# Optimization experiments

Hardware: AMD Instinct MI355X
Metric: run time of the kernel (lower is better)

The kernel has to match this reference:

```python
import jax, jax.numpy as jnp
import numpy as np

B, G, C = 8, 512, 32  # batch, grid size, channel width (INIT_DIM)
NPB = 32768           # nonzeros per batch element


def _sconv(x, k, stride, pad):
    # dense conv; sparse semantics recovered by masking with the output
    # coordinate occupancy (Minkowski conv only produces active outputs)
    return jax.lax.conv_general_dilated(
        x, k, (stride, stride), [(pad, pad), (pad, pad)],
        dimension_numbers=('NHWC', 'HWIO', 'NHWC'))


def _downsample_mask(m):
    # ME strided output coord exists iff any input coord in the 2x2 cell is active
    return jax.lax.reduce_window(m, 0.0, jax.lax.max, (1, 2, 2, 1), (1, 2, 2, 1), 'VALID')


def setup_inputs() -> dict:
    key = jax.random.key(0)
    ks = jax.random.split(key, 16)
    b = jnp.repeat(jnp.arange(B, dtype=jnp.int32), NPB)
    yx = jax.random.randint(ks[0], (B * NPB, 2), 0, G, dtype=jnp.int32)
    coords = jnp.concatenate([b[:, None], yx], axis=1)          # [N,3] (b,y,x)
    feats = jax.random.normal(ks[1], (B * NPB, 1), jnp.float32)  # 1 feature/nnz
    x2 = jax.random.normal(ks[2], (B, 3), jnp.float32)
    # Minkowski conv kernels (bias=False by default); HWIO layout
    K1 = jax.random.normal(ks[3], (5, 5, 1, C), jnp.float32) * 0.28   # kaiming-ish
    K2 = jax.random.normal(ks[4], (3, 3, C, C), jnp.float32) * 0.083
    K3 = jax.random.normal(ks[5], (3, 3, C, C), jnp.float32) * 0.083
    K4 = jax.random.normal(ks[6], (3, 3, C, C), jnp.float32) * 0.083
    # feature MLP: Linear(3,64) -> ReLU -> Linear(64,32)
    W1 = jax.random.normal(ks[7], (3, 64), jnp.float32) * 0.3
    b1 = jnp.zeros((64,), jnp.float32)
    W2 = jax.random.normal(ks[8], (64, 32), jnp.float32) * 0.25
    b2 = jnp.zeros((32,), jnp.float32)
    # matrix_embedding: Linear(64,128) -> ReLU
    W3 = jax.random.normal(ks[9], (64, 128), jnp.float32) * 0.18
    b3 = jnp.zeros((128,), jnp.float32)
    return {'coords': coords, 'feats': feats, 'x2': x2,
            'K1': K1, 'K2': K2, 'K3': K3, 'K4': K4,
            'W1': W1, 'b1': b1, 'W2': W2, 'b2': b2, 'W3': W3, 'b3': b3}


def reference(coords, feats, x2, K1, K2, K3, K4, W1, b1, W2, b2, W3, b3):
    bi, yi, xi = coords[:, 0], coords[:, 1], coords[:, 2]
    grid = jnp.zeros((B, G, G, 1), jnp.float32).at[bi, yi, xi, 0].set(feats[:, 0])
    m1 = jnp.zeros((B, G, G, 1), jnp.float32).at[bi, yi, xi, 0].set(1.0)
    # layer1: k=5 s=1 (output coords == input coords)
    y1 = jax.nn.relu(_sconv(grid, K1, 1, 2)) * m1
    # layers 2-4: k=3 s=2; centered at even positions, masked by strided occupancy
    m2 = _downsample_mask(m1)
    y2 = jax.nn.relu(_sconv(y1, K2, 2, 1)) * m2
    m3 = _downsample_mask(m2)
    y3 = jax.nn.relu(_sconv(y2, K3, 2, 1)) * m3
    m4 = _downsample_mask(m3)
    y4 = jax.nn.relu(_sconv(y3, K4, 2, 1)) * m4
    # global average pool over active output coordinates per batch
    cnt = jnp.sum(m4, axis=(1, 2))                      # [B,1]
    pooled = jnp.sum(y4, axis=(1, 2)) / jnp.maximum(cnt, 1.0)  # [B,32]
    # aux feature MLP
    h = jax.nn.relu(x2[:, :3] @ W1 + b1) @ W2 + b2      # [B,32]
    z = jnp.concatenate([pooled, h], axis=1)            # [B,64]
    return jax.nn.relu(z @ W3 + b3)                     # [B,128]
```

## Files before the change

kernel.cpp:

```cpp
#include <hip/hip_runtime.h>
#include <hip/hip_bf16.h>
#include <stdint.h>


static constexpr int G_ = 512;
static constexpr int NPTS = 8 * 32768;

#define DEVI __device__ __forceinline__

typedef __attribute__((ext_vector_type(8))) short bf16x8;
typedef __attribute__((ext_vector_type(4))) float f32x4;
typedef __attribute__((ext_vector_type(4))) unsigned u32x4;

DEVI float bf_lo(unsigned w) { return __uint_as_float(w << 16); }
DEVI float bf_hi(unsigned w) { return __uint_as_float(w & 0xFFFF0000u); }
DEVI unsigned comp(const uint4& v, int i) {
  return i == 0 ? v.x : i == 1 ? v.y : i == 2 ? v.z : v.w;
}
DEVI unsigned short f2bf_bits(float f) {
  unsigned u = __float_as_uint(f);
  unsigned r = u + 0x7FFFu + ((u >> 16) & 1u);
  return (unsigned short)(r >> 16);
}

__global__ __launch_bounds__(256) void k_scatter(const int* __restrict__ coords,
                                                 int* __restrict__ idxg) {
  int i = blockIdx.x * 256 + threadIdx.x;
  if (i >= NPTS) return;
  int b = coords[3 * i], y = coords[3 * i + 1], x = coords[3 * i + 2];
  atomicMax(&idxg[((size_t)b * G_ + y) * G_ + x], i);
}

__global__ __launch_bounds__(256) void k_grid(const int* __restrict__ idxg,
                                              const float* __restrict__ feats,
                                              unsigned* __restrict__ grid2) {
  int i = blockIdx.x * 256 + threadIdx.x;
  int v = idxg[i];
  float f = (v >= 0) ? feats[v] : 0.0f;
  unsigned short hb = f2bf_bits(f);
  unsigned short lb = f2bf_bits(f - __uint_as_float((unsigned)hb << 16));
  grid2[i] = (unsigned)hb | ((unsigned)lb << 16);
}

__global__ __launch_bounds__(256) void k_packw(
    const float* __restrict__ K1f, const float* __restrict__ K2,
    const float* __restrict__ K3, const float* __restrict__ K4,
    unsigned short* __restrict__ pw1h, unsigned short* __restrict__ pw1l,
    unsigned short* __restrict__ pw2, unsigned short* __restrict__ pw3,
    unsigned short* __restrict__ pw4) {
  const int t = threadIdx.x;
  if (t < 128) {
    int h = t >> 6, ln = t & 63;
    int g2 = ln >> 4, co = h * 16 + (ln & 15);
#pragma unroll
    for (int j = 0; j < 8; j++) {
      int k = 8 * g2 + j;
      float v = (k < 25) ? K1f[k * 32 + co] : 0.f;
      unsigned short hb = f2bf_bits(v);
      pw1h[t * 8 + j] = hb;
      pw1l[t * 8 + j] = f2bf_bits(v - __uint_as_float((unsigned)hb << 16));
    }
  }
  const float* Ks[3] = {K2, K3, K4};
  unsigned short* ps[3] = {pw2, pw3, pw4};
  for (int m = 0; m < 3; m++)
    for (int e = t; e < 1152; e += 256) {
      int kk = e >> 7, rem = e & 127;
      int h = rem >> 6, ln = rem & 63;
      int g2 = ln >> 4, co = h * 16 + (ln & 15);
#pragma unroll
      for (int j = 0; j < 8; j++)
        ps[m][e * 8 + j] = f2bf_bits(Ks[m][((kk * 32) + 8 * g2 + j) * 32 + co]);
    }
}

__global__ __launch_bounds__(256) void k_masks(const int* __restrict__ idxg,
                                               float* __restrict__ m2,
                                               float* __restrict__ m3,
                                               float* __restrict__ m4) {
  __shared__ float sm2[32][32];
  __shared__ float sm3[16][16];
  const int b = blockIdx.z, ty0 = blockIdx.y * 32, tx0 = blockIdx.x * 32;
  const int t = threadIdx.x;
  for (int i = t; i < 1024; i += 256) {
    int r = i >> 5, c = i & 31;
    const int* p = idxg + ((size_t)b * 512 + 2 * (ty0 + r)) * 512 + 2 * (tx0 + c);
    float v = ((p[0] & p[1] & p[512] & p[513]) >= 0) ? 1.f : 0.f;
    m2[((size_t)b * 256 + ty0 + r) * 256 + tx0 + c] = v;
    sm2[r][c] = v;
  }
  __syncthreads();
  {
    int r = t >> 4, c = t & 15;
    float v = fmaxf(fmaxf(sm2[2 * r][2 * c], sm2[2 * r][2 * c + 1]),
                    fmaxf(sm2[2 * r + 1][2 * c], sm2[2 * r + 1][2 * c + 1]));
    m3[((size_t)b * 128 + (ty0 >> 1) + r) * 128 + (tx0 >> 1) + c] = v;
    sm3[r][c] = v;
  }
  __syncthreads();
  if (t < 64) {
    int r = t >> 3, c = t & 7;
    float v = fmaxf(fmaxf(sm3[2 * r][2 * c], sm3[2 * r][2 * c + 1]),
                    fmaxf(sm3[2 * r + 1][2 * c], sm3[2 * r + 1][2 * c + 1]));
    m4[((size_t)b * 64 + (ty0 >> 2) + r) * 64 + (tx0 >> 2) + c] = v;
  }
}

__global__ __launch_bounds__(256) void k_conv1_mfma(
    const unsigned* __restrict__ grid2, const int* __restrict__ idxg,
    const unsigned short* __restrict__ pw1h,
    const unsigned short* __restrict__ pw1l,
    __hip_bfloat16* __restrict__ y1) {
  constexpr int PITCH = 264;
  __shared__ unsigned s_tile[8 * PITCH];
  const int t = threadIdx.x;
  const int b = blockIdx.z, R = blockIdx.y * 4, x0 = blockIdx.x * 256;
  for (int i = t; i < 8 * 260; i += 256) {
    int rr = i / 260, cc = i - rr * 260;
    int gy = R - 2 + rr, gx = x0 - 2 + cc;
    unsigned v = 0;
    if (gy >= 0 && gy < G_ && gx >= 0 && gx < G_)
      v = grid2[((size_t)b * G_ + gy) * G_ + gx];
    s_tile[rr * PITCH + cc] = v;
  }

  const int lane = t & 63, w = t >> 6;
  const int r = lane & 15, g = lane >> 4;
  bf16x8 bh[2], bl[2];
#pragma unroll
  for (int h = 0; h < 2; h++) {
    bh[h] = *(const bf16x8*)&pw1h[(h * 64 + lane) * 8];
    bl[h] = *(const bf16x8*)&pw1l[(h * 64 + lane) * 8];
  }
  int toff[8]; bool tval[8];
#pragma unroll
  for (int j = 0; j < 8; j++) {
    int k = 8 * g + j;
    tval[j] = (k < 25);
    int kq = tval[j] ? k : 0;
    int ky = kq / 5, kx = kq - 5 * ky;
    toff[j] = (w + ky) * PITCH + kx;
  }
  __syncthreads();

  const int oy = R + w;
  const size_t rowo = ((size_t)b * G_ + oy) * G_;

  for (int s = 0; s < 16; s++) {
    const int oxl = s * 16;
    unsigned wv[8];
#pragma unroll
    for (int j = 0; j < 8; j++)
      wv[j] = tval[j] ? s_tile[toff[j] + oxl + r] : 0u;
    u32x4 ua, ul;
#pragma unroll
    for (int p = 0; p < 4; p++) {
      unsigned w0 = wv[2 * p], w1 = wv[2 * p + 1];
      ua[p] = (w0 & 0xffffu) | (w1 << 16);
      ul[p] = (w0 >> 16) | (w1 & 0xffff0000u);
    }
    bf16x8 ahv = __builtin_bit_cast(bf16x8, ua);
    bf16x8 alv = __builtin_bit_cast(bf16x8, ul);
    f32x4 acc0 = {0.f, 0.f, 0.f, 0.f}, acc1 = {0.f, 0.f, 0.f, 0.f};
    acc0 = __builtin_amdgcn_mfma_f32_16x16x32_bf16(ahv, bh[0], acc0, 0, 0, 0);
    acc1 = __builtin_amdgcn_mfma_f32_16x16x32_bf16(ahv, bh[1], acc1, 0, 0, 0);
    acc0 = __builtin_amdgcn_mfma_f32_16x16x32_bf16(ahv, bl[0], acc0, 0, 0, 0);
    acc1 = __builtin_amdgcn_mfma_f32_16x16x32_bf16(ahv, bl[1], acc1, 0, 0, 0);
    acc0 = __builtin_amdgcn_mfma_f32_16x16x32_bf16(alv, bh[0], acc0, 0, 0, 0);
    acc1 = __builtin_amdgcn_mfma_f32_16x16x32_bf16(alv, bh[1], acc1, 0, 0, 0);

#pragma unroll
    for (int q = 0; q < 4; q++) {
      const size_t opix = rowo + (x0 + oxl + g * 4 + q);
      const float m = (idxg[opix] >= 0) ? 1.f : 0.f;
      unsigned short* op = (unsigned short*)(y1 + opix * 32);
      op[r] = f2bf_bits(fmaxf(acc0[q], 0.f) * m);
      op[r + 16] = f2bf_bits(fmaxf(acc1[q], 0.f) * m);
    }
  }
}

template <int HI, int SEGS, int NW>
__global__ __launch_bounds__(NW * 64) void k_conv3x3s2_mfma(
    const __hip_bfloat16* __restrict__ in,
    const unsigned short* __restrict__ pw,
    const float* __restrict__ mask, __hip_bfloat16* __restrict__ out) {
  constexpr int WI = HI, HO = HI / 2, WO = WI / 2;
  constexpr int NSEG = WO / 16 / SEGS;
  const int t = threadIdx.x;
  const int lane = t & 63, w = t >> 6;
  const int r = lane & 15, g = lane >> 4;
  bf16x8 bw[9][2];
#pragma unroll
  for (int kk = 0; kk < 9; kk++)
#pragma unroll
    for (int h = 0; h < 2; h++)
      bw[kk][h] = *(const bf16x8*)&pw[((kk * 2 + h) * 64 + lane) * 8];

  const int b = blockIdx.z;
  const int oy = blockIdx.y * NW + w;
  const int ox_base = blockIdx.x * (WO / SEGS);
  const __hip_bfloat16* inb = in + (size_t)b * HI * WI * 32;

  for (int s = 0; s < NSEG; s++) {
    const int ox0 = ox_base + s * 16;
    f32x4 acc0 = {0.f, 0.f, 0.f, 0.f}, acc1 = {0.f, 0.f, 0.f, 0.f};
#pragma unroll
    for (int ky = 0; ky < 3; ky++) {
      const int iy = 2 * oy + ky - 1;
      const __hip_bfloat16* rowp = inb + (size_t)(iy < 0 ? 0 : iy) * WI * 32;
#pragma unroll
      for (int kx = 0; kx < 3; kx++) {
        const int ix = 2 * (ox0 + r) + kx - 1;
        uint4 v = *(const uint4*)(rowp + (size_t)(ix < 0 ? 0 : ix) * 32 + g * 8);
        if ((iy | ix) < 0) { v.x = 0; v.y = 0; v.z = 0; v.w = 0; }
        bf16x8 a = *reinterpret_cast<const bf16x8*>(&v);
        acc0 = __builtin_amdgcn_mfma_f32_16x16x32_bf16(a, bw[ky * 3 + kx][0],
                                                       acc0, 0, 0, 0);
        acc1 = __builtin_amdgcn_mfma_f32_16x16x32_bf16(a, bw[ky * 3 + kx][1],
                                                       acc1, 0, 0, 0);
      }
    }
    const size_t rowo = ((size_t)b * HO + oy) * WO;
#pragma unroll
    for (int q = 0; q < 4; q++) {
      const size_t opix = rowo + (ox0 + g * 4 + q);
      const float m = mask[opix];
      unsigned short* op = (unsigned short*)(out + opix * 32);
      op[r] = f2bf_bits(fmaxf(acc0[q], 0.f) * m);
      op[r + 16] = f2bf_bits(fmaxf(acc1[q], 0.f) * m);
    }
  }
}

__global__ __launch_bounds__(256) void k_pool(const __hip_bfloat16* __restrict__ y4,
                                              const float* __restrict__ m4,
                                              float* __restrict__ pooled) {
  const int b = blockIdx.x, t = threadIdx.x;
  const int c8 = t & 3, g = t >> 2;
  float s[8] = {0, 0, 0, 0, 0, 0, 0, 0};
  for (int p = g; p < 4096; p += 64) {
    uint4 raw = *(const uint4*)(y4 + ((size_t)b * 4096 + p) * 32 + c8 * 8);
#pragma unroll
    for (int cp = 0; cp < 4; cp++) {
      unsigned w = comp(raw, cp);
      s[2 * cp] += bf_lo(w);
      s[2 * cp + 1] += bf_hi(w);
    }
  }
  __shared__ float s_red[64][32];
  __shared__ float s_cnt[256];
#pragma unroll
  for (int j = 0; j < 8; j++) s_red[g][c8 * 8 + j] = s[j];
  float cnt = 0;
  for (int p = t; p < 4096; p += 256) cnt += m4[(size_t)b * 4096 + p];
  s_cnt[t] = cnt;
  __syncthreads();
  for (int st = 32; st > 0; st >>= 1) {
    if (g < st) {
#pragma unroll
      for (int j = 0; j < 8; j++) s_red[g][c8 * 8 + j] += s_red[g + st][c8 * 8 + j];
    }
    __syncthreads();
  }
  for (int st = 128; st > 0; st >>= 1) {
    if (t < st) s_cnt[t] += s_cnt[t + st];
    __syncthreads();
  }
  if (t < 32) pooled[b * 32 + t] = s_red[0][t] / fmaxf(s_cnt[0], 1.f);
}

__global__ __launch_bounds__(256) void k_mlp(
    const float* __restrict__ pooled, const float* __restrict__ x2,
    const float* __restrict__ W1, const float* __restrict__ b1,
    const float* __restrict__ W2, const float* __restrict__ b2,
    const float* __restrict__ W3, const float* __restrict__ b3,
    float* __restrict__ outp) {
  __shared__ float s_h1[8 * 64];
  __shared__ float s_z[8 * 64];
  const int t = threadIdx.x;
  for (int i = t; i < 512; i += 256) {
    int bb = i >> 6, j = i & 63;
    float a = b1[j] + x2[bb * 3 + 0] * W1[0 * 64 + j] +
              x2[bb * 3 + 1] * W1[1 * 64 + j] + x2[bb * 3 + 2] * W1[2 * 64 + j];
    s_h1[i] = fmaxf(a, 0.f);
  }
  __syncthreads();
  {
    int bb = t >> 5, ci = t & 31;
    float a = b2[ci];
    for (int k = 0; k < 64; k++) a += s_h1[bb * 64 + k] * W2[k * 32 + ci];
    s_z[bb * 64 + 32 + ci] = a;
    s_z[bb * 64 + ci] = pooled[bb * 32 + ci];
  }
  __syncthreads();
  for (int o = t; o < 1024; o += 256) {
    int bb = o >> 7, j = o & 127;
    float a = b3[j];
    for (int k = 0; k < 64; k++) a += s_z[bb * 64 + k] * W3[k * 128 + j];
    outp[o] = fmaxf(a, 0.f);
  }
}

extern "C" void kernel_launch(void* const* d_in, const int* in_sizes, int n_in,
                              void* d_out, int out_size, void* d_ws,
                              size_t ws_size, hipStream_t stream) {
  const int* coords = (const int*)d_in[0];
  const float* feats = (const float*)d_in[1];
  const float* x2 = (const float*)d_in[2];
  const float* K1 = (const float*)d_in[3];
  const float* K2 = (const float*)d_in[4];
  const float* K3 = (const float*)d_in[5];
  const float* K4 = (const float*)d_in[6];
  const float* W1 = (const float*)d_in[7];
  const float* b1 = (const float*)d_in[8];
  const float* W2 = (const float*)d_in[9];
  const float* b2 = (const float*)d_in[10];
  const float* W3 = (const float*)d_in[11];
  const float* b3 = (const float*)d_in[12];
  float* outp = (float*)d_out;

  char* ws = (char*)d_ws;
  size_t off = 0;
  auto alloc = [&](size_t bytes) {
    char* p = ws + off;
    off += (bytes + 255) & ~(size_t)255;
    return p;
  };
  int* idxg = (int*)alloc(8ull * 512 * 512 * 4);
  unsigned* grid2 = (unsigned*)alloc(8ull * 512 * 512 * 4);
  __hip_bfloat16* y1 = (__hip_bfloat16*)alloc(8ull * 512 * 512 * 32 * 2);
  __hip_bfloat16* y2 = (__hip_bfloat16*)alloc(8ull * 256 * 256 * 32 * 2);
  __hip_bfloat16* y3 = (__hip_bfloat16*)alloc(8ull * 128 * 128 * 32 * 2);
  __hip_bfloat16* y4 = (__hip_bfloat16*)alloc(8ull * 64 * 64 * 32 * 2);
  float* m2 = (float*)alloc(8ull * 256 * 256 * 4);
  float* m3 = (float*)alloc(8ull * 128 * 128 * 4);
  float* m4 = (float*)alloc(8ull * 64 * 64 * 4);
  float* pooled = (float*)alloc(8 * 32 * 4);
  unsigned short* pw1h = (unsigned short*)alloc(128 * 8 * 2);
  unsigned short* pw1l = (unsigned short*)alloc(128 * 8 * 2);
  unsigned short* pw2 = (unsigned short*)alloc(1152 * 8 * 2);
  unsigned short* pw3 = (unsigned short*)alloc(1152 * 8 * 2);
  unsigned short* pw4 = (unsigned short*)alloc(1152 * 8 * 2);
  (void)ws_size; (void)in_sizes; (void)n_in; (void)out_size;

  hipMemsetAsync(idxg, 0xFF, 8ull * 512 * 512 * 4, stream);

  k_packw<<<1, 256, 0, stream>>>(K1, K2, K3, K4, pw1h, pw1l, pw2, pw3, pw4);
  k_scatter<<<NPTS / 256, 256, 0, stream>>>(coords, idxg);
  k_grid<<<(8 * 512 * 512) / 256, 256, 0, stream>>>(idxg, feats, grid2);
  k_masks<<<dim3(8, 8, 8), 256, 0, stream>>>(idxg, m2, m3, m4);

  k_conv1_mfma<<<dim3(2, 128, 8), 256, 0, stream>>>(grid2, idxg, pw1h, pw1l, y1);

  k_conv3x3s2_mfma<512, 2, 4><<<dim3(2, 64, 8), 256, 0, stream>>>(y1, pw2, m2, y2);
  k_conv3x3s2_mfma<256, 2, 4><<<dim3(2, 32, 8), 256, 0, stream>>>(y2, pw3, m3, y3);
  k_conv3x3s2_mfma<128, 4, 1><<<dim3(4, 64, 8), 64, 0, stream>>>(y3, pw4, m4, y4);

  k_pool<<<8, 256, 0, stream>>>(y4, m4, pooled);
  k_mlp<<<1, 256, 0, stream>>>(pooled, x2, W1, b1, W2, b2, W3, b3, outp);
}
```

Baseline: 237.1 us.

## Fuse conv1 and conv2 through shared memory, eliminating y1 global round trip

Conv1 (5x5) and the first strided 3x3 conv now run in one kernel. Each block computes a 17x33 tile of y1 (with halo) into swizzled LDS, masks it, then runs conv2 directly from LDS, so the 128MB bf16 y1 tensor is never written to or read from global memory. Weight packing is changed to an interleaved channel order so each lane writes two adjacent bf16 channels as one 32-bit store, and that packed store is also used in the remaining convs. In exchange, the halo rows and columns of y1 are recomputed by neighbouring blocks, and the larger LDS footprint limits occupancy.

Measured after the change: 226.8 us. 4.3% less time.

```diff
diff --git a/kernel.cpp b/kernel.cpp
--- a/kernel.cpp
+++ b/kernel.cpp
@@ -21,6 +21,9 @@
   unsigned u = __float_as_uint(f);
   unsigned r = u + 0x7FFFu + ((u >> 16) & 1u);
   return (unsigned short)(r >> 16);
+}
+DEVI unsigned pack2(float a, float b) {
+  return (unsigned)f2bf_bits(a) | ((unsigned)f2bf_bits(b) << 16);
 }
 
 __global__ __launch_bounds__(256) void k_scatter(const int* __restrict__ coords,
@@ -51,7 +54,7 @@
   const int t = threadIdx.x;
   if (t < 128) {
     int h = t >> 6, ln = t & 63;
-    int g2 = ln >> 4, co = h * 16 + (ln & 15);
+    int g2 = ln >> 4, co = 2 * (ln & 15) + h;
 #pragma unroll
     for (int j = 0; j < 8; j++) {
       int k = 8 * g2 + j;
@@ -67,7 +70,7 @@
     for (int e = t; e < 1152; e += 256) {
       int kk = e >> 7, rem = e & 127;
       int h = rem >> 6, ln = rem & 63;
-      int g2 = ln >> 4, co = h * 16 + (ln & 15);
+      int g2 = ln >> 4, co = 2 * (ln & 15) + h;
 #pragma unroll
       for (int j = 0; j < 8; j++)
         ps[m][e * 8 + j] = f2bf_bits(Ks[m][((kk * 32) + 8 * g2 + j) * 32 + co]);
@@ -106,52 +109,74 @@
   }
 }
 
-__global__ __launch_bounds__(256) void k_conv1_mfma(
+__global__ __launch_bounds__(256, 3) void k_conv12(
     const unsigned* __restrict__ grid2, const int* __restrict__ idxg,
     const unsigned short* __restrict__ pw1h,
     const unsigned short* __restrict__ pw1l,
-    __hip_bfloat16* __restrict__ y1) {
-  constexpr int PITCH = 264;
-  __shared__ unsigned s_tile[8 * PITCH];
+    const unsigned short* __restrict__ pw2, const float* __restrict__ m2,
+    __hip_bfloat16* __restrict__ y2) {
+  __shared__ unsigned s_grid[21 * 40];
+  __shared__ unsigned short s_m1[17 * 34];
+  __shared__ unsigned short s_y1[17 * 33 * 32];
+
   const int t = threadIdx.x;
-  const int b = blockIdx.z, R = blockIdx.y * 4, x0 = blockIdx.x * 256;
-  for (int i = t; i < 8 * 260; i += 256) {
-    int rr = i / 260, cc = i - rr * 260;
-    int gy = R - 2 + rr, gx = x0 - 2 + cc;
+  const int b = blockIdx.z, by = blockIdx.y, bx = blockIdx.x;
+  const int gyb = 16 * by - 3, gxb = 32 * bx - 3;
+  const size_t ibase = (size_t)b * G_ * G_;
+
+  for (int i = t; i < 21 * 37; i += 256) {
+    int rr = i / 37, cc = i - rr * 37;
+    int gy = gyb + rr, gx = gxb + cc;
     unsigned v = 0;
     if (gy >= 0 && gy < G_ && gx >= 0 && gx < G_)
-      v = grid2[((size_t)b * G_ + gy) * G_ + gx];
-    s_tile[rr * PITCH + cc] = v;
+      v = grid2[ibase + (size_t)gy * G_ + gx];
+    s_grid[rr * 40 + cc] = v;
+  }
+  for (int i = t; i < 17 * 33; i += 256) {
+    int rr = i / 33, cc = i - rr * 33;
+    int gy = gyb + 2 + rr, gx = gxb + 2 + cc;
+    unsigned short mv = 0;
+    if (gy >= 0 && gy < G_ && gx >= 0 && gx < G_)
+      mv = (idxg[ibase + (size_t)gy * G_ + gx] >= 0) ? 1 : 0;
+    s_m1[rr * 34 + cc] = mv;
   }
 
   const int lane = t & 63, w = t >> 6;
   const int r = lane & 15, g = lane >> 4;
-  bf16x8 bh[2], bl[2];
+
+  bf16x8 b1h[2], b1l[2];
 #pragma unroll
   for (int h = 0; h < 2; h++) {
-    bh[h] = *(const bf16x8*)&pw1h[(h * 64 + lane) * 8];
-    bl[h] = *(const bf16x8*)&pw1l[(h * 64 + lane) * 8];
-  }
-  int toff[8]; bool tval[8];
+    b1h[h] = *(const bf16x8*)&pw1h[(h * 64 + lane) * 8];
+    b1l[h] = *(const bf16x8*)&pw1l[(h * 64 + lane) * 8];
+  }
+  bf16x8 bw2[9][2];
+#pragma unroll
+  for (int kk = 0; kk < 9; kk++)
+#pragma unroll
+    for (int h = 0; h < 2; h++)
+      bw2[kk][h] = *(const bf16x8*)&pw2[((kk * 2 + h) * 64 + lane) * 8];
+
+  int reloff[8]; bool tval[8];
 #pragma unroll
   for (int j = 0; j < 8; j++) {
     int k = 8 * g + j;
     tval[j] = (k < 25);
     int kq = tval[j] ? k : 0;
-    int ky = kq / 5, kx = kq - 5 * ky;
-    toff[j] = (w + ky) * PITCH + kx;
-  }
-  __syncthreads();
-
-  const int oy = R + w;
-  const size_t rowo = ((size_t)b * G_ + oy) * G_;
-
-  for (int s = 0; s < 16; s++) {
-    const int oxl = s * 16;
+    reloff[j] = (kq / 5) * 40 + (kq % 5);
+  }
+
+  __syncthreads();
+
+  for (int seg = w; seg < 36; seg += 4) {
+    int piy, pix;
+    if (seg < 34) { piy = seg >> 1; pix = ((seg & 1) << 4) + r; }
+    else          { piy = (seg - 34) + r; pix = 32; }
+    const int tapb = piy * 40 + pix;
     unsigned wv[8];
 #pragma unroll
     for (int j = 0; j < 8; j++)
-      wv[j] = tval[j] ? s_tile[toff[j] + oxl + r] : 0u;
+      wv[j] = tval[j] ? s_grid[tapb + reloff[j]] : 0u;
     u32x4 ua, ul;
 #pragma unroll
     for (int p = 0; p < 4; p++) {
@@ -162,20 +187,54 @@
     bf16x8 ahv = __builtin_bit_cast(bf16x8, ua);
     bf16x8 alv = __builtin_bit_cast(bf16x8, ul);
     f32x4 acc0 = {0.f, 0.f, 0.f, 0.f}, acc1 = {0.f, 0.f, 0.f, 0.f};
-    acc0 = __builtin_amdgcn_mfma_f32_16x16x32_bf16(ahv, bh[0], acc0, 0, 0, 0);
-    acc1 = __builtin_amdgcn_mfma_f32_16x16x32_bf16(ahv, bh[1], acc1, 0, 0, 0);
-    acc0 = __builtin_amdgcn_mfma_f32_16x16x32_bf16(ahv, bl[0], acc0, 0, 0, 0);
-    acc1 = __builtin_amdgcn_mfma_f32_16x16x32_bf16(ahv, bl[1], acc1, 0, 0, 0);
-    acc0 = __builtin_amdgcn_mfma_f32_16x16x32_bf16(alv, bh[0], acc0, 0, 0, 0);
-    acc1 = __builtin_amdgcn_mfma_f32_16x16x32_bf16(alv, bh[1], acc1, 0, 0, 0);
-
+    acc0 = __builtin_amdgcn_mfma_f32_16x16x32_bf16(ahv, b1h[0], acc0, 0, 0, 0);
+    acc1 = __builtin_amdgcn_mfma_f32_16x16x32_bf16(ahv, b1h[1], acc1, 0, 0, 0);
+    acc0 = __builtin_amdgcn_mfma_f32_16x16x32_bf16(ahv, b1l[0], acc0, 0, 0, 0);
+    acc1 = __builtin_amdgcn_mfma_f32_16x16x32_bf16(ahv, b1l[1], acc1, 0, 0, 0);
+    acc0 = __builtin_amdgcn_mfma_f32_16x16x32_bf16(alv, b1h[0], acc0, 0, 0, 0);
+    acc1 = __builtin_amdgcn_mfma_f32_16x16x32_bf16(alv, b1h[1], acc1, 0, 0, 0);
 #pragma unroll
     for (int q = 0; q < 4; q++) {
-      const size_t opix = rowo + (x0 + oxl + g * 4 + q);
-      const float m = (idxg[opix] >= 0) ? 1.f : 0.f;
-      unsigned short* op = (unsigned short*)(y1 + opix * 32);
-      op[r] = f2bf_bits(fmaxf(acc0[q], 0.f) * m);
-      op[r + 16] = f2bf_bits(fmaxf(acc1[q], 0.f) * m);
+      const int m = g * 4 + q;
+      int eiy, eix;
+      if (seg < 34) { eiy = seg >> 1; eix = ((seg & 1) << 4) + m; }
+      else          { eiy = (seg - 34) + m; eix = 32; }
+      float mk = (float)s_m1[eiy * 34 + eix];
+      unsigned ov = pack2(fmaxf(acc0[q], 0.f) * mk, fmaxf(acc1[q], 0.f) * mk);
+      int slot = eiy * 33 + eix;
+      unsigned byo = (unsigned)(slot * 64 + 4 * r) ^
+                     ((((unsigned)slot >> 1) & 7u) << 4);
+      *(unsigned*)((char*)s_y1 + byo) = ov;
+    }
+  }
+  __syncthreads();
+
+  const int ty0 = 8 * by, tx0 = 16 * bx;
+  for (int oy = w; oy < 8; oy += 4) {
+    f32x4 acc0 = {0.f, 0.f, 0.f, 0.f}, acc1 = {0.f, 0.f, 0.f, 0.f};
+#pragma unroll
+    for (int ky = 0; ky < 3; ky++) {
+      const int iy = 2 * oy + ky;
+#pragma unroll
+      for (int kx = 0; kx < 3; kx++) {
+        const int slot = iy * 33 + 2 * r + kx;
+        unsigned byo = (unsigned)(slot * 64 + g * 16) ^
+                       ((((unsigned)slot >> 1) & 7u) << 4);
+        bf16x8 a = *(const bf16x8*)((char*)s_y1 + byo);
+        acc0 = __builtin_amdgcn_mfma_f32_16x16x32_bf16(a, bw2[ky * 3 + kx][0],
+                                                       acc0, 0, 0, 0);
+        acc1 = __builtin_amdgcn_mfma_f32_16x16x32_bf16(a, bw2[ky * 3 + kx][1],
+                                                       acc1, 0, 0, 0);
+      }
+    }
+    const size_t rowo = ((size_t)b * 256 + ty0 + oy) * 256;
+#pragma unroll
+    for (int q = 0; q < 4; q++) {
+      const int m = g * 4 + q;
+      const size_t opix = rowo + tx0 + m;
+      const float mk = m2[opix];
+      unsigned ov = pack2(fmaxf(acc0[q], 0.f) * mk, fmaxf(acc1[q], 0.f) * mk);
+      *(unsigned*)(y2 + opix * 32 + 2 * r) = ov;
     }
   }
 }
@@ -226,9 +285,8 @@
     for (int q = 0; q < 4; q++) {
       const size_t opix = rowo + (ox0 + g * 4 + q);
       const float m = mask[opix];
-      unsigned short* op = (unsigned short*)(out + opix * 32);
-      op[r] = f2bf_bits(fmaxf(acc0[q], 0.f) * m);
-      op[r + 16] = f2bf_bits(fmaxf(acc1[q], 0.f) * m);
+      unsigned ov = pack2(fmaxf(acc0[q], 0.f) * m, fmaxf(acc1[q], 0.f) * m);
+      *(unsigned*)(out + opix * 32 + 2 * r) = ov;
     }
   }
 }
@@ -329,7 +387,6 @@
   };
   int* idxg = (int*)alloc(8ull * 512 * 512 * 4);
   unsigned* grid2 = (unsigned*)alloc(8ull * 512 * 512 * 4);
-  __hip_bfloat16* y1 = (__hip_bfloat16*)alloc(8ull * 512 * 512 * 32 * 2);
   __hip_bfloat16* y2 = (__hip_bfloat16*)alloc(8ull * 256 * 256 * 32 * 2);
   __hip_bfloat16* y3 = (__hip_bfloat16*)alloc(8ull * 128 * 128 * 32 * 2);
   __hip_bfloat16* y4 = (__hip_bfloat16*)alloc(8ull * 64 * 64 * 32 * 2);
@@ -351,9 +408,9 @@
   k_grid<<<(8 * 512 * 512) / 256, 256, 0, stream>>>(idxg, feats, grid2);
   k_masks<<<dim3(8, 8, 8), 256, 0, stream>>>(idxg, m2, m3, m4);
 
-  k_conv1_mfma<<<dim3(2, 128, 8), 256, 0, stream>>>(grid2, idxg, pw1h, pw1l, y1);
-
-  k_conv3x3s2_mfma<512, 2, 4><<<dim3(2, 64, 8), 256, 0, stream>>>(y1, pw2, m2, y2);
+  k_conv12<<<dim3(16, 32, 8), 256, 0, stream>>>(grid2, idxg, pw1h, pw1l, pw2,
+                                                m2, y2);
+
   k_conv3x3s2_mfma<256, 2, 4><<<dim3(2, 32, 8), 256, 0, stream>>>(y2, pw3, m3, y3);
   k_conv3x3s2_mfma<128, 4, 1><<<dim3(4, 64, 8), 64, 0, stream>>>(y3, pw4, m4, y4);
 
```
